# Performance work log

Measured on AMD Instinct MI355X. Metric: run time of the kernel, lower is better.

## Reference

```python
import jax, jax.numpy as jnp
import numpy as np

H, C, D, F = 8, 1024, 128, 512  # num_heads, num_chanels, out_dim, featurs_dim
B = 16


def setup_inputs() -> dict:
    key = jax.random.key(0)
    ks = jax.random.split(key, 9)
    s = 0.02
    return {
        "x": jax.random.normal(ks[0], (B, C, F), jnp.float32),
        "Wk": jax.random.normal(ks[1], (F, H * D), jnp.float32) * s,
        "bk": jax.random.normal(ks[2], (H * D,), jnp.float32) * s,
        "Wq": jax.random.normal(ks[3], (F, H * D), jnp.float32) * s,
        "bq": jax.random.normal(ks[4], (H * D,), jnp.float32) * s,
        "Wv": jax.random.normal(ks[5], (F, H * D), jnp.float32) * s,
        "bv": jax.random.normal(ks[6], (H * D,), jnp.float32) * s,
        "Ww0": jax.random.normal(ks[7], (H * D, D), jnp.float32) * s,
        "bw0": jax.random.normal(ks[8], (D,), jnp.float32) * s,
    }


def reference(x, Wk, bk, Wq, bq, Wv, bv, Ww0, bw0):
    # Linear projections on last dim: [B, C, H*D]
    # NOTE: the original reshapes [B, C, H*D] -> [B, H, C, D] WITHOUT a permute,
    # which mixes channel/head axes; we replicate that exactly.
    k = (x @ Wk + bk).reshape(-1, H, C, D)
    q = (x @ Wq + bq).reshape(-1, H, C, D)
    v = (x @ Wv + bv).reshape(-1, H, C, D)
    scores = jnp.einsum('bhcf,bhdf->bhcd', q, k) / jnp.sqrt(jnp.float32(D))
    att = jax.nn.softmax(scores, axis=-1) - jnp.eye(C, dtype=scores.dtype)
    vals = jnp.einsum('bhcd,bhdf->bhcf', att, v)          # [B, H, C, D]
    vals = vals.transpose(0, 2, 1, 3).reshape(vals.shape[0], C, H * D)
    return vals @ Ww0 + bw0                                # [B, C, D]
```

## Files before the change

### kernel.cpp

```cpp
#include <hip/hip_runtime.h>
#include <hip/hip_bf16.h>
#include <cstdint>
#include <cstddef>

using u16 = unsigned short;
typedef __attribute__((ext_vector_type(4))) float f32x4;
typedef __attribute__((ext_vector_type(16))) float f32x16;
typedef __attribute__((ext_vector_type(8))) unsigned short u16x8;
typedef __attribute__((ext_vector_type(4))) unsigned short u16x4;
typedef __attribute__((ext_vector_type(4))) unsigned int u32x4;
typedef __bf16 bfrag __attribute__((ext_vector_type(8)));

constexpr int Hn = 8, Cn = 1024, Dn = 128, Fn = 512, Bn = 16;
constexpr int M1 = Bn * Cn;

constexpr size_t OFF_XB  = 0;
constexpr size_t SZ_XB   = (size_t)M1 * Fn * 2;
constexpr size_t OFF_WT  = OFF_XB + SZ_XB;
constexpr size_t SZ_WT   = 3ull * 1024 * 512 * 2;
constexpr size_t OFF_W0T = OFF_WT + SZ_WT;
constexpr size_t SZ_W0T  = 128ull * 1024 * 2;
constexpr size_t OFF_Q   = OFF_W0T + SZ_W0T;
constexpr size_t SZ_P    = (size_t)Bn * Hn * Cn * Dn * 2;
constexpr size_t OFF_K   = OFF_Q + SZ_P;
constexpr size_t OFF_V   = OFF_K + SZ_P;
constexpr size_t OFF_ATT = OFF_V + SZ_P;

__device__ __forceinline__ float bf2f(u16 u) {
  unsigned int x = ((unsigned int)u) << 16;
  return __builtin_bit_cast(float, x);
}
__device__ __forceinline__ u16 f2bf(float f) {
  unsigned int u = __builtin_bit_cast(unsigned int, f);
  u += 0x7fffu + ((u >> 16) & 1u);
  return (u16)(u >> 16);
}
__device__ __forceinline__ f32x4 mfma16(bfrag a, bfrag b, f32x4 c) {
  return __builtin_amdgcn_mfma_f32_16x16x32_bf16(a, b, c, 0, 0, 0);
}
__device__ __forceinline__ f32x16 mfma32(bfrag a, bfrag b, f32x16 c) {
  return __builtin_amdgcn_mfma_f32_32x32x16_bf16(a, b, c, 0, 0, 0);
}
__device__ __forceinline__ void gload16(const void* g, void* lds) {
  __builtin_amdgcn_global_load_lds(
      (const __attribute__((address_space(1))) unsigned int*)g,
      (__attribute__((address_space(3))) unsigned int*)lds, 16, 0, 0);
}
__device__ __forceinline__ unsigned cvtpk(float lo, float hi) {
  unsigned r;
  asm("v_cvt_pk_bf16_f32 %0, %1, %2" : "=v"(r) : "v"(lo), "v"(hi));
  return r;
}
__device__ __forceinline__ float fexp2(float x) {
  float r;
  asm("v_exp_f32 %0, %1" : "=v"(r) : "v"(x));
  return r;
}

__global__ void cvt_bf16(const float* __restrict__ in, u16* __restrict__ out, int n) {
  int idx = (blockIdx.x * blockDim.x + threadIdx.x) * 4;
  if (idx < n) {
    float4 v = *(const float4*)(in + idx);
    u16x4 o;
    o.x = f2bf(v.x); o.y = f2bf(v.y); o.z = f2bf(v.z); o.w = f2bf(v.w);
    *(u16x4*)(out + idx) = o;
  }
}

__global__ void transpose_cvt(const float* __restrict__ in, u16* __restrict__ out,
                              int R, int Cc) {
  __shared__ float tile[32][33];
  int c0 = blockIdx.x * 32, r0 = blockIdx.y * 32;
  int tx = threadIdx.x, ty = threadIdx.y;
#pragma unroll
  for (int i = 0; i < 4; ++i)
    tile[ty + i * 8][tx] = in[(size_t)(r0 + ty + i * 8) * Cc + c0 + tx];
  __syncthreads();
#pragma unroll
  for (int i = 0; i < 4; ++i)
    out[(size_t)(c0 + ty + i * 8) * R + r0 + tx] = f2bf(tile[tx][ty + i * 8]);
}

__global__ void transpose_cvt3(const float* __restrict__ W0, const float* __restrict__ W1,
                               const float* __restrict__ W2, u16* __restrict__ out) {
  __shared__ float tile[32][33];
  const int z = blockIdx.z;
  const float* in = (z == 0) ? W0 : (z == 1) ? W1 : W2;
  u16* op = out + (size_t)z * 1024 * 512;
  int c0 = blockIdx.x * 32, r0 = blockIdx.y * 32;
  int tx = threadIdx.x, ty = threadIdx.y;
#pragma unroll
  for (int i = 0; i < 4; ++i)
    tile[ty + i * 8][tx] = in[(size_t)(r0 + ty + i * 8) * 1024 + c0 + tx];
  __syncthreads();
#pragma unroll
  for (int i = 0; i < 4; ++i)
    op[(size_t)(c0 + ty + i * 8) * 512 + r0 + tx] = f2bf(tile[tx][ty + i * 8]);
}

__global__ void vtrans(const u16* __restrict__ in, u16* __restrict__ out) {
  __shared__ u16 tile[32][33];
  int d0 = blockIdx.x * 32, c0 = blockIdx.y * 32, bh = blockIdx.z;
  const u16* ip = in + (size_t)bh * (Cn * Dn);
  u16* op = out + (size_t)bh * (Dn * Cn);
  int tx = threadIdx.x, ty = threadIdx.y;
#pragma unroll
  for (int i = 0; i < 4; ++i)
    tile[ty + i * 8][tx] = ip[(size_t)(c0 + ty + i * 8) * Dn + d0 + tx];
  __syncthreads();
#pragma unroll
  for (int i = 0; i < 4; ++i)
    op[(size_t)(d0 + ty + i * 8) * Cn + c0 + tx] = tile[tx][ty + i * 8];
}

__global__ void qkv_gemm(const u16* __restrict__ xb, const u16* __restrict__ wt,
                         const float* __restrict__ bq, const float* __restrict__ bk,
                         const float* __restrict__ bv,
                         u16* __restrict__ qout, u16* __restrict__ kout,
                         u16* __restrict__ vout) {
  __shared__ u16 As[128 * 64];
  __shared__ u16 Bs[128 * 64];
  const int m0 = blockIdx.x * 128;
  const int n0 = blockIdx.y * 128;
  const int p  = blockIdx.z;
  const u16* wp = wt + (size_t)p * 1024 * 512;
  const float* bias = (p == 0) ? bq : (p == 1) ? bk : bv;
  u16* outp = (p == 0) ? qout : (p == 1) ? kout : vout;
  const float osc = (p == 0) ? 0.12751744116389548f : 1.0f;

  const int tid = threadIdx.x, l = tid & 63, w = tid >> 6;
  const int lr = l & 15, lg = l >> 4;
  const int wr = w >> 1, wc = w & 1;

  f32x4 acc[4][4] = {};

  for (int kt = 0; kt < Fn; kt += 64) {
#pragma unroll
    for (int i = 0; i < 4; ++i) {
      int chb = (i * 4 + w) * 64;
      int ch = chb + l;
      int row = ch >> 3, scc = (ch & 7) ^ (row & 7);
      gload16(xb + (size_t)(m0 + row) * Fn + kt + scc * 8, &As[chb * 8]);
    }
#pragma unroll
    for (int i = 0; i < 4; ++i) {
      int chb = (i * 4 + w) * 64;
      int ch = chb + l;
      int row = ch >> 3, scc = (ch & 7) ^ (row & 7);
      gload16(wp + (size_t)(n0 + row) * Fn + kt + scc * 8, &Bs[chb * 8]);
    }
    __syncthreads();
#pragma unroll
    for (int kk = 0; kk < 2; ++kk) {
      bfrag af[4], bf_[4];
#pragma unroll
      for (int fm = 0; fm < 4; ++fm) {
        int row = wr * 64 + fm * 16 + lr;
        int off = (kk * 4 + lg) ^ (row & 7);
        af[fm] = *(const bfrag*)&As[row * 64 + off * 8];
      }
#pragma unroll
      for (int fn = 0; fn < 4; ++fn) {
        int row = wc * 64 + fn * 16 + lr;
        int off = (kk * 4 + lg) ^ (row & 7);
        bf_[fn] = *(const bfrag*)&Bs[row * 64 + off * 8];
      }
#pragma unroll
      for (int fm = 0; fm < 4; ++fm)
#pragma unroll
        for (int fn = 0; fn < 4; ++fn)
          acc[fm][fn] = mfma16(af[fm], bf_[fn], acc[fm][fn]);
    }
    __syncthreads();
  }

#pragma unroll
  for (int fm = 0; fm < 4; ++fm) {
#pragma unroll
    for (int r = 0; r < 4; ++r) {
      int m = m0 + wr * 64 + fm * 16 + lg * 4 + r;
      int b = m >> 10, c = m & 1023;
      int gh = c >> 7;
#pragma unroll
      for (int fn = 0; fn < 4; ++fn) {
        int j = n0 + wc * 64 + fn * 16 + lr;
        float v = (acc[fm][fn][r] + bias[j]) * osc;
        int ii = ((c & 127) << 3) | (j >> 7);
        int d = j & 127;
        size_t idx = (((size_t)(b * 8 + gh) * 1024 + ii) << 7) | d;
        outp[idx] = f2bf(v);
      }
    }
  }
}

__global__ __launch_bounds__(512, 2)
void attn_kernel(const u16* __restrict__ qp_all, const u16* __restrict__ kp_all,
                 const u16* __restrict__ vt_all, u16* __restrict__ attout) {
  __shared__ u16 smem[2 * 16384];
  char* smb = (char*)smem;

  const int bid = blockIdx.x;
  const int wg = (bid & 7) * 64 + (bid >> 3);
  const int bh = wg >> 2;
  const int qtp = wg & 3;

  const int tid = threadIdx.x, l = tid & 63, w = tid >> 6;
  const int q31 = l & 31, hi = l >> 5;

  const u16* qp  = qp_all + (size_t)bh * (Cn * Dn);
  const u16* kp  = kp_all + (size_t)bh * (Cn * Dn);
  const u16* vtp = vt_all + (size_t)bh * (Dn * Cn);
  const int qr0 = qtp * 256 + w * 32;

  const unsigned LK = (unsigned)(q31 * 256) ^ (unsigned)((q31 & 15) * 16) ^ (unsigned)(hi * 16);
  const unsigned LV = 16384u ^ (unsigned)(q31 * 128) ^ (unsigned)((q31 & 7) * 16) ^ (unsigned)(hi * 16);

  const u16* ksrc[2]; const u16* vsrc[2];
  unsigned kdst[2], vdst[2];
#pragma unroll
  for (int c = 0; c < 2; ++c) {
    int ch = c * 512 + tid;
    int krow = ch >> 4, kscc = (ch & 15) ^ (krow & 15);
    ksrc[c] = kp + krow * 128 + kscc * 8;
    int vrow = ch >> 3, vscc = (ch & 7) ^ (vrow & 7);
    vsrc[c] = vtp + (size_t)vrow * 1024 + vscc * 8;
    kdst[c] = (unsigned)((c * 512 + w * 64) * 16);
    vdst[c] = 16384u + (unsigned)((c * 512 + w * 64) * 16);
  }
  auto stage = [&](int t2, unsigned bufb) {
#pragma unroll
    for (int c = 0; c < 2; ++c)
      gload16(ksrc[c] + (size_t)t2 * 8192, smb + (bufb ^ kdst[c]));
#pragma unroll
    for (int c = 0; c < 2; ++c)
      gload16(vsrc[c] + (size_t)t2 * 64, smb + (bufb ^ vdst[c]));
  };

  bfrag aq[8];
#pragma unroll
  for (int kk = 0; kk < 8; ++kk)
    aq[kk] = *(const bfrag*)(qp + (size_t)(qr0 + q31) * Dn + kk * 16 + hi * 8);

  f32x16 ot[4] = {};
  float lsum = 0.f;

  stage(0, 0);
  __syncthreads();

  unsigned bufb = 0;
  for (int t = 0; t < 16; ++t) {
    const unsigned nb = bufb ^ 32768u;
    if (t < 15) stage(t + 1, nb);
    const unsigned LKb = LK ^ bufb;
    const unsigned LVb = LV ^ bufb;

    f32x16 st0 = {}, st1 = {};
    __builtin_amdgcn_s_setprio(1);
#pragma unroll
    for (int kk = 0; kk < 8; ++kk) {
      bfrag k0 = *(const bfrag*)(smb + (LKb ^ (unsigned)(kk * 32)));
      st0 = mfma32(k0, aq[kk], st0);
      bfrag k1 = *(const bfrag*)(smb + (LKb ^ (unsigned)(8192 + kk * 32)));
      st1 = mfma32(k1, aq[kk], st1);
    }
    __builtin_amdgcn_s_setprio(0);

    float rp[4] = {0.f, 0.f, 0.f, 0.f};
#pragma unroll
    for (int r = 0; r < 16; ++r) {
      float p0 = fexp2(st0[r]);
      st0[r] = p0;
      rp[r & 3] += p0;
    }
#pragma unroll
    for (int r = 0; r < 16; ++r) {
      float p1 = fexp2(st1[r]);
      st1[r] = p1;
      rp[r & 3] += p1;
    }
    lsum += (rp[0] + rp[1]) + (rp[2] + rp[3]);

    bfrag pb[4];
    {
      unsigned c0_[8], c1_[8];
#pragma unroll
      for (int m = 0; m < 8; ++m) {
        c0_[m] = cvtpk(st0[2 * m], st0[2 * m + 1]);
        c1_[m] = cvtpk(st1[2 * m], st1[2 * m + 1]);
      }
#pragma unroll
      for (int kkt = 0; kkt < 2; ++kkt) {
        unsigned a0 = c0_[4 * kkt + 0], b0 = c0_[4 * kkt + 2];
        unsigned a1 = c0_[4 * kkt + 1], b1 = c0_[4 * kkt + 3];
        asm("v_permlane32_swap_b32 %0, %1" : "+v"(a0), "+v"(b0));
        asm("v_permlane32_swap_b32 %0, %1" : "+v"(a1), "+v"(b1));
        u32x4 bw; bw.x = a0; bw.y = a1; bw.z = b0; bw.w = b1;
        pb[kkt] = __builtin_bit_cast(bfrag, bw);
      }
#pragma unroll
      for (int kkt = 0; kkt < 2; ++kkt) {
        unsigned a0 = c1_[4 * kkt + 0], b0 = c1_[4 * kkt + 2];
        unsigned a1 = c1_[4 * kkt + 1], b1 = c1_[4 * kkt + 3];
        asm("v_permlane32_swap_b32 %0, %1" : "+v"(a0), "+v"(b0));
        asm("v_permlane32_swap_b32 %0, %1" : "+v"(a1), "+v"(b1));
        u32x4 bw; bw.x = a0; bw.y = a1; bw.z = b0; bw.w = b1;
        pb[2 + kkt] = __builtin_bit_cast(bfrag, bw);
      }
    }

    __builtin_amdgcn_s_setprio(1);
#pragma unroll
    for (int kk = 0; kk < 4; ++kk) {
#pragma unroll
      for (int dt = 0; dt < 4; ++dt) {
        bfrag vf = *(const bfrag*)(smb + (LVb ^ (unsigned)(dt * 4096 + kk * 32)));
        ot[dt] = mfma32(vf, pb[kk], ot[dt]);
      }
    }
    __builtin_amdgcn_s_setprio(0);
    __syncthreads();
    bufb = nb;
  }

  const float lfull = lsum + __shfl_xor(lsum, 32, 64);
  const float linv = 1.f / lfull;
  const int c1 = qr0 + q31;
  u16* my = smem + w * 4096;
#pragma unroll
  for (int dt = 0; dt < 4; ++dt)
#pragma unroll
    for (int rp2 = 0; rp2 < 8; ++rp2) {
      int reg = 2 * rp2;
      int d = dt * 32 + (reg & 3) + 8 * (reg >> 2) + 4 * hi;
      float v0 = bf2f(vtp[((size_t)d << 10) | c1]);
      float v1 = bf2f(vtp[((size_t)(d + 1) << 10) | c1]);
      unsigned pk = cvtpk(ot[dt][reg] * linv - v0, ot[dt][reg + 1] * linv - v1);
      *(unsigned*)&my[q31 * 128 + (((d >> 3) ^ (q31 & 7)) << 3) + (d & 7)] = pk;
    }
  const int b = bh >> 3, h = bh & 7;
#pragma unroll
  for (int it = 0; it < 8; ++it) {
    int rowq = it * 4 + (l >> 4);
    int ch = l & 15;
    u16x8 rd = *(const u16x8*)&my[rowq * 128 + ((ch ^ (rowq & 7))) * 8];
    int cg = qr0 + rowq;
    *(u16x8*)&attout[(((size_t)(b * 1024 + cg)) * 8 + h) * 128 + ch * 8] = rd;
  }
}

__global__ void out_gemm(const u16* __restrict__ A, const u16* __restrict__ Bt,
                         const float* __restrict__ bias, float* __restrict__ out) {
  __shared__ u16 As[32 * 64];
  __shared__ u16 Bs[128 * 64];
  const int m0 = blockIdx.x * 32;
  const int tid = threadIdx.x, l = tid & 63, w = tid >> 6;
  const int lr = l & 15, lg = l >> 4;
  f32x4 acc[2][2] = {};

  for (int kt = 0; kt < 1024; kt += 64) {
    {
      int ch = w * 64 + l;
      int row = ch >> 3, scc = (ch & 7) ^ (row & 7);
      gload16(A + (size_t)(m0 + row) * 1024 + kt + scc * 8, &As[(w * 64) * 8]);
    }
#pragma unroll
    for (int i = 0; i < 4; ++i) {
      int chb = (i * 4 + w) * 64;
      int ch = chb + l;
      int row = ch >> 3, scc = (ch & 7) ^ (row & 7);
      gload16(Bt + (size_t)row * 1024 + kt + scc * 8, &Bs[chb * 8]);
    }
    __syncthreads();
#pragma unroll
    for (int kk = 0; kk < 2; ++kk) {
      bfrag af[2], bf_[2];
#pragma unroll
      for (int fm = 0; fm < 2; ++fm) {
        int row = fm * 16 + lr;
        int off = (kk * 4 + lg) ^ (row & 7);
        af[fm] = *(const bfrag*)&As[row * 64 + off * 8];
      }
#pragma unroll
      for (int fn = 0; fn < 2; ++fn) {
        int row = w * 32 + fn * 16 + lr;
        int off = (kk * 4 + lg) ^ (row & 7);
        bf_[fn] = *(const bfrag*)&Bs[row * 64 + off * 8];
      }
#pragma unroll
      for (int fm = 0; fm < 2; ++fm)
#pragma unroll
        for (int fn = 0; fn < 2; ++fn)
          acc[fm][fn] = mfma16(af[fm], bf_[fn], acc[fm][fn]);
    }
    __syncthreads();
  }
#pragma unroll
  for (int fm = 0; fm < 2; ++fm)
#pragma unroll
    for (int r = 0; r < 4; ++r) {
      int m = m0 + fm * 16 + lg * 4 + r;
#pragma unroll
      for (int fn = 0; fn < 2; ++fn) {
        int j = w * 32 + fn * 16 + lr;
        out[(size_t)m * 128 + j] = acc[fm][fn][r] + bias[j];
      }
    }
}

extern "C" void kernel_launch(void* const* d_in, const int* in_sizes, int n_in,
                              void* d_out, int out_size, void* d_ws, size_t ws_size,
                              hipStream_t stream) {
  const float* x   = (const float*)d_in[0];
  const float* Wk  = (const float*)d_in[1];
  const float* bk_ = (const float*)d_in[2];
  const float* Wq  = (const float*)d_in[3];
  const float* bq_ = (const float*)d_in[4];
  const float* Wv  = (const float*)d_in[5];
  const float* bv_ = (const float*)d_in[6];
  const float* Ww0 = (const float*)d_in[7];
  const float* bw0 = (const float*)d_in[8];
  float* out = (float*)d_out;

  char* ws = (char*)d_ws;
  u16* xb   = (u16*)(ws + OFF_XB);
  u16* wt   = (u16*)(ws + OFF_WT);
  u16* w0t  = (u16*)(ws + OFF_W0T);
  u16* qpm  = (u16*)(ws + OFF_Q);
  u16* kpm  = (u16*)(ws + OFF_K);
  u16* vpm  = (u16*)(ws + OFF_V);
  u16* attb = (u16*)(ws + OFF_ATT);

  cvt_bf16<<<(M1 * Fn / 4 + 255) / 256, 256, 0, stream>>>(x, xb, M1 * Fn);
  dim3 tb(32, 8);
  transpose_cvt3<<<dim3(32, 16, 3), tb, 0, stream>>>(Wq, Wk, Wv, wt);
  transpose_cvt<<<dim3(4, 32), tb, 0, stream>>>(Ww0, w0t, 1024, 128);

  qkv_gemm<<<dim3(128, 8, 3), 256, 0, stream>>>(xb, wt, bq_, bk_, bv_, qpm, kpm, attb);

  vtrans<<<dim3(4, 32, 128), tb, 0, stream>>>(attb, vpm);

  attn_kernel<<<dim3(512), 512, 0, stream>>>(qpm, kpm, vpm, attb);

  out_gemm<<<512, 256, 0, stream>>>(attb, w0t, bw0, out);
}
```

Measured before the change: 178.3 us.

## Pipeline QKV GEMM with triple-buffered async loads and larger 128x256 tiles

Restructures the QKV projection GEMM to use 128x256 tiles with 512 threads, a three-stage shared-memory ring buffer, and prefetching two K-steps ahead with explicit vmcnt waits instead of full syncthreads. It also remaps block IDs to group work per XCD, and raises wave priority around the MFMA bursts. The aim is to hide global-load latency behind matrix math and increase reuse of A tiles. In exchange it uses about 144KB of LDS, limiting occupancy to one block per CU, and depends on hand-written wait counts being correct.

```diff
diff --git a/kernel.cpp b/kernel.cpp
--- a/kernel.cpp
+++ b/kernel.cpp
@@ -113,16 +113,21 @@
     op[(size_t)(d0 + ty + i * 8) * Cn + c0 + tx] = tile[tx][ty + i * 8];
 }
 
-__global__ void qkv_gemm(const u16* __restrict__ xb, const u16* __restrict__ wt,
-                         const float* __restrict__ bq, const float* __restrict__ bk,
-                         const float* __restrict__ bv,
-                         u16* __restrict__ qout, u16* __restrict__ kout,
-                         u16* __restrict__ vout) {
-  __shared__ u16 As[128 * 64];
-  __shared__ u16 Bs[128 * 64];
-  const int m0 = blockIdx.x * 128;
-  const int n0 = blockIdx.y * 128;
-  const int p  = blockIdx.z;
+__global__ __launch_bounds__(512, 1)
+void qkv_gemm(const u16* __restrict__ xb, const u16* __restrict__ wt,
+              const float* __restrict__ bq, const float* __restrict__ bk,
+              const float* __restrict__ bv,
+              u16* __restrict__ qout, u16* __restrict__ kout,
+              u16* __restrict__ vout) {
+  __shared__ u16 smem[3 * 24576];
+  char* smb = (char*)smem;
+
+  const int bid = blockIdx.x;
+  const int wg = (bid & 7) * 192 + (bid >> 3);
+  const int mt = wg / 12, yz = wg % 12;
+  const int y = yz / 3, p = yz - y * 3;
+  const int m0 = mt * 128, n0 = y * 256;
+
   const u16* wp = wt + (size_t)p * 1024 * 512;
   const float* bias = (p == 0) ? bq : (p == 1) ? bk : bv;
   u16* outp = (p == 0) ? qout : (p == 1) ? kout : vout;
@@ -130,48 +135,67 @@
 
   const int tid = threadIdx.x, l = tid & 63, w = tid >> 6;
   const int lr = l & 15, lg = l >> 4;
-  const int wr = w >> 1, wc = w & 1;
+  const int wr = w >> 2, wc = w & 3;
+
+  const u16* asrc[2]; unsigned adst[2];
+#pragma unroll
+  for (int c = 0; c < 2; ++c) {
+    int ch = c * 512 + tid, row = ch >> 3, scc = (ch & 7) ^ (row & 7);
+    asrc[c] = xb + (size_t)(m0 + row) * 512 + scc * 8;
+    adst[c] = (unsigned)(ch * 16);
+  }
+  const u16* bsrc[4]; unsigned bdst[4];
+#pragma unroll
+  for (int c = 0; c < 4; ++c) {
+    int ch = c * 512 + tid, row = ch >> 3, scc = (ch & 7) ^ (row & 7);
+    bsrc[c] = wp + (size_t)(n0 + row) * 512 + scc * 8;
+    bdst[c] = (unsigned)(16384 + ch * 16);
+  }
+  auto stage = [&](int t, int b) {
+    char* base = smb + b * 49152;
+#pragma unroll
+    for (int c = 0; c < 2; ++c) gload16(asrc[c] + t * 64, base + adst[c]);
+#pragma unroll
+    for (int c = 0; c < 4; ++c) gload16(bsrc[c] + t * 64, base + bdst[c]);
+  };
 
   f32x4 acc[4][4] = {};
 
-  for (int kt = 0; kt < Fn; kt += 64) {
-#pragma unroll
-    for (int i = 0; i < 4; ++i) {
-      int chb = (i * 4 + w) * 64;
-      int ch = chb + l;
-      int row = ch >> 3, scc = (ch & 7) ^ (row & 7);
-      gload16(xb + (size_t)(m0 + row) * Fn + kt + scc * 8, &As[chb * 8]);
-    }
-#pragma unroll
-    for (int i = 0; i < 4; ++i) {
-      int chb = (i * 4 + w) * 64;
-      int ch = chb + l;
-      int row = ch >> 3, scc = (ch & 7) ^ (row & 7);
-      gload16(wp + (size_t)(n0 + row) * Fn + kt + scc * 8, &Bs[chb * 8]);
-    }
-    __syncthreads();
+  stage(0, 0);
+  stage(1, 1);
+  asm volatile("s_waitcnt vmcnt(6)" ::: "memory");
+  __builtin_amdgcn_s_barrier();
+
+  for (int t = 0; t < 8; ++t) {
+    const char* Ab = smb + (t % 3) * 49152;
+    const char* Bb = Ab + 16384;
+    if (t < 6) stage(t + 2, (t + 2) % 3);
+
 #pragma unroll
     for (int kk = 0; kk < 2; ++kk) {
       bfrag af[4], bf_[4];
 #pragma unroll
       for (int fm = 0; fm < 4; ++fm) {
         int row = wr * 64 + fm * 16 + lr;
-        int off = (kk * 4 + lg) ^ (row & 7);
-        af[fm] = *(const bfrag*)&As[row * 64 + off * 8];
+        af[fm] = *(const bfrag*)(Ab + row * 128 + (((kk * 4 + lg) ^ (row & 7)) * 16));
       }
 #pragma unroll
       for (int fn = 0; fn < 4; ++fn) {
         int row = wc * 64 + fn * 16 + lr;
-        int off = (kk * 4 + lg) ^ (row & 7);
-        bf_[fn] = *(const bfrag*)&Bs[row * 64 + off * 8];
-      }
+        bf_[fn] = *(const bfrag*)(Bb + row * 128 + (((kk * 4 + lg) ^ (row & 7)) * 16));
+      }
+      __builtin_amdgcn_s_setprio(1);
 #pragma unroll
       for (int fm = 0; fm < 4; ++fm)
 #pragma unroll
         for (int fn = 0; fn < 4; ++fn)
           acc[fm][fn] = mfma16(af[fm], bf_[fn], acc[fm][fn]);
-    }
-    __syncthreads();
+      __builtin_amdgcn_s_setprio(0);
+    }
+
+    if (t < 6)      asm volatile("s_waitcnt vmcnt(6)" ::: "memory");
+    else if (t == 6) asm volatile("s_waitcnt vmcnt(0)" ::: "memory");
+    if (t < 7) __builtin_amdgcn_s_barrier();
   }
 
 #pragma unroll
@@ -436,7 +460,7 @@
   transpose_cvt3<<<dim3(32, 16, 3), tb, 0, stream>>>(Wq, Wk, Wv, wt);
   transpose_cvt<<<dim3(4, 32), tb, 0, stream>>>(Ww0, w0t, 1024, 128);
 
-  qkv_gemm<<<dim3(128, 8, 3), 256, 0, stream>>>(xb, wt, bq_, bk_, bv_, qpm, kpm, attb);
+  qkv_gemm<<<dim3(1536), 512, 0, stream>>>(xb, wt, bq_, bk_, bv_, qpm, kpm, attb);
 
   vtrans<<<dim3(4, 32, 128), tb, 0, stream>>>(attb, vpm);
 
```

New measurement: 195.2 us. 9.5% more time.
